# Kernel tuning notes

Hardware: AMD Instinct MI355X
Metric: run time of the kernel (lower is better)

## Reference

```python
import jax, jax.numpy as jnp
import numpy as np

S = 512      # seq_len -> S*S - S edges
V = 32000    # vocab_size
D = 128      # d_model
H = 4        # num_heads
L = 2        # num_layers
DN = 64      # d_node
DE = 64      # d_edge
DF = 4 * D   # ffn hidden
TEMP = 1.0   # temperature_init
E = S * S - S


def setup_inputs() -> dict:
    key = jax.random.key(0)
    ks = jax.random.split(key, 12)
    n = lambda k, shp: jax.random.normal(k, shp, dtype=jnp.float32) * 0.02
    return {
        "token_ids": jax.random.randint(ks[0], (S,), 0, V),
        "u": jax.random.uniform(ks[1], (E,), dtype=jnp.float32),
        "emb": n(ks[2], (V, D)),
        "Wqkv": n(ks[3], (L, D, 3 * D)), "bqkv": jnp.zeros((L, 3 * D)),
        "Wo": n(ks[4], (L, D, D)), "bo": jnp.zeros((L, D)),
        "ln1_g": jnp.ones((L, D)), "ln1_b": jnp.zeros((L, D)),
        "Wff1": n(ks[5], (L, D, DF)), "bff1": jnp.zeros((L, DF)),
        "Wff2": n(ks[6], (L, DF, D)), "bff2": jnp.zeros((L, D)),
        "ln2_g": jnp.ones((L, D)), "ln2_b": jnp.zeros((L, D)),
        "node_W": n(ks[7], (D, DN)), "node_b": jnp.zeros((DN,)),
        "sc_W1": n(ks[8], (2 * D + 1, D)), "sc_b1": jnp.zeros((D,)),
        "sc_W2": n(ks[9], (D, 1)), "sc_b2": jnp.zeros((1,)),
        "te_W": n(ks[10], (2 * D + 1, DE)), "te_b": jnp.zeros((DE,)),
    }


def _layernorm(x, g, b):
    m = jnp.mean(x, -1, keepdims=True)
    v = jnp.var(x, -1, keepdims=True)
    return (x - m) * jax.lax.rsqrt(v + 1e-5) * g + b


def _pos_encoding(s, d):
    pos = jnp.arange(s, dtype=jnp.float32)[:, None]
    div = jnp.exp(jnp.arange(0, d, 2, dtype=jnp.float32) * (-np.log(10000.0) / d))
    pe = jnp.zeros((s, d), dtype=jnp.float32)
    pe = pe.at[:, 0::2].set(jnp.sin(pos * div)).at[:, 1::2].set(jnp.cos(pos * div))
    return pe


_SRC_NP = np.repeat(np.arange(S), S)
_TGT_NP = np.tile(np.arange(S), S)
_KEEP = _SRC_NP != _TGT_NP
SRC = jnp.asarray(_SRC_NP[_KEEP])  # [E] static off-diagonal indices
TGT = jnp.asarray(_TGT_NP[_KEEP])


def _forward(token_ids, u, emb, Wqkv, bqkv, Wo, bo, ln1_g, ln1_b, Wff1, bff1,
             Wff2, bff2, ln2_g, ln2_b, node_W, node_b, sc_W1, sc_b1, sc_W2,
             sc_b2, te_W, te_b):
    # --- mini transformer backbone ---
    x = emb[token_ids] + _pos_encoding(S, D)  # [S, D]
    dh = D // H
    for l in range(L):
        qkv = x @ Wqkv[l] + bqkv[l]
        q, k, v = jnp.split(qkv, 3, axis=-1)
        q = q.reshape(S, H, dh); k = k.reshape(S, H, dh); v = v.reshape(S, H, dh)
        scores = jnp.einsum('qhd,khd->hqk', q, k) / np.sqrt(dh).astype(np.float32)
        attn = jax.nn.softmax(scores, axis=-1)
        o = jnp.einsum('hqk,khd->qhd', attn, v).reshape(S, D)
        x = _layernorm(x + o @ Wo[l] + bo[l], ln1_g[l], ln1_b[l])
        h = jax.nn.gelu(x @ Wff1[l] + bff1[l], approximate=False)
        x = _layernorm(x + h @ Wff2[l] + bff2[l], ln2_g[l], ln2_b[l])
    node_features = x @ node_W + node_b  # [S, DN]
    # --- all-pairs edge construction (off-diagonal) ---
    pos_diff = ((SRC - TGT).astype(jnp.float32) / S)[:, None]  # [E, 1]
    pair = jnp.concatenate([x[SRC], x[TGT], pos_diff], axis=-1)  # [E, 2D+1]
    # edge scorer MLP
    hs = jax.nn.gelu(pair @ sc_W1 + sc_b1, approximate=False)
    edge_logits = (hs @ sc_W2 + sc_b2)[:, 0]  # [E]
    # gumbel-sigmoid (soft, hard=False)
    uu = jnp.clip(u, 1e-8, 1.0 - 1e-8)
    gnoise = -jnp.log(-jnp.log(uu))
    edge_gates = jax.nn.sigmoid((edge_logits + gnoise) / TEMP)  # [E]
    # gated edge features
    edge_feats = (pair @ te_W + te_b) * edge_gates[:, None]  # [E, DE]
    return node_features, edge_feats, edge_gates


def reference(token_ids, u, emb, Wqkv, bqkv, Wo, bo, ln1_g, ln1_b, Wff1, bff1,
              Wff2, bff2, ln2_g, ln2_b, node_W, node_b, sc_W1, sc_b1, sc_W2,
              sc_b2, te_W, te_b):
    node_features, edge_feats, edge_gates = _forward(
        token_ids, u, emb, Wqkv, bqkv, Wo, bo, ln1_g, ln1_b, Wff1, bff1,
        Wff2, bff2, ln2_g, ln2_b, node_W, node_b, sc_W1, sc_b1, sc_W2,
        sc_b2, te_W, te_b)
    edge_index = jnp.stack([SRC, TGT])  # [2, E]
    return node_features, edge_feats, edge_index, edge_gates
```

## Files before the change

kernel.cpp:

```cpp
#include <hip/hip_runtime.h>
#include <math.h>

#define SS 512
#define DD 128
#define HH 4
#define DHH 32
#define DFF 512
#define E_EDGES 261632

__device__ __forceinline__ float gelu_f(float v) {
    return 0.5f * v * (1.0f + erff(v * 0.70710678118654752f));
}
__device__ __forceinline__ float fgelu(float x) {
    float x2 = x * x;
    float z = x * fmaf(-0.0713548164f, x2, -1.5957691216f);
    float e = __expf(z);
    return x * __builtin_amdgcn_rcpf(1.0f + e);
}

template<int DO_EMBED>
__global__ __launch_bounds__(384) void k_qkv(const float* __restrict__ xin,
                                             const int* __restrict__ tok,
                                             const float* __restrict__ emb,
                                             float* __restrict__ xout,
                                             const float* __restrict__ W,
                                             const float* __restrict__ b,
                                             float* __restrict__ qkv) {
    __shared__ float xs[DD];
    int row = blockIdx.x;
    int c = threadIdx.x;
    if (DO_EMBED) {
        if (c < 128) {
            float v = emb[(size_t)tok[row] * DD + c];
            int i2 = (c >> 1) << 1;
            float div = expf(-(float)i2 * (9.210340371976184f / 128.0f));
            float arg = (float)row * div;
            v += (c & 1) ? cosf(arg) : sinf(arg);
            xs[c] = v;
            xout[row * DD + c] = v;
        }
    } else {
        if (c < 128) xs[c] = xin[row * DD + c];
    }
    __syncthreads();
    float a = b[c];
    #pragma unroll 4
    for (int d = 0; d < DD; ++d) a = fmaf(xs[d], W[d * 384 + c], a);
    qkv[row * 384 + c] = a;
}

template<int DO_NODE>
__global__ __launch_bounds__(1024) void k_attn_tail(const float* __restrict__ qkv,
                                                    float* __restrict__ x,
                                                    const float* __restrict__ Wo,
                                                    const float* __restrict__ bo,
                                                    const float* __restrict__ g1,
                                                    const float* __restrict__ b1,
                                                    const float* __restrict__ W1,
                                                    const float* __restrict__ bf1,
                                                    const float* __restrict__ W2,
                                                    const float* __restrict__ bf2,
                                                    const float* __restrict__ g2,
                                                    const float* __restrict__ b2,
                                                    const float* __restrict__ nodeW,
                                                    const float* __restrict__ nodeb,
                                                    const float* __restrict__ scW1,
                                                    const float* __restrict__ scb1,
                                                    const float* __restrict__ teW,
                                                    const float* __restrict__ teb,
                                                    float* __restrict__ out_node,
                                                    float* __restrict__ As,
                                                    float* __restrict__ Atp,
                                                    float* __restrict__ Bs,
                                                    float* __restrict__ Btp) {
    int r0 = blockIdx.x * 2;
    int tid = threadIdx.x;
    int wave = tid >> 6, lane = tid & 63;
    __shared__ float sq[2][DD];
    __shared__ float ps[2][HH][SS];
    __shared__ float smax[2][HH][4], ssum[2][HH][4];
    __shared__ float opart[2][HH][4][DHH];
    __shared__ float os[2][DD];
    __shared__ float pred4[4][2][DD];
    __shared__ float x1[2][DD];
    __shared__ float hhl[2][DFF];
    __shared__ float xf[2][DD];
    __shared__ float red[2][2];
    if (tid < 256) sq[tid >> 7][tid & 127] = qkv[(r0 + (tid >> 7)) * 384 + (tid & 127)];
    __syncthreads();
    const float scale = 0.17677669529663687f;
    int h = wave & 3, kh = wave >> 2;
    int k0 = kh * 128 + lane, k1 = k0 + 64;
    float s00 = 0, s01 = 0, s10 = 0, s11 = 0;
    {
        const float4* kp0 = reinterpret_cast<const float4*>(&qkv[(size_t)k0 * 384 + 128 + h * DHH]);
        const float4* kp1 = reinterpret_cast<const float4*>(&qkv[(size_t)k1 * 384 + 128 + h * DHH]);
        #pragma unroll
        for (int i = 0; i < 8; ++i) {
            float4 a = kp0[i], bq = kp1[i];
            int d0 = h * DHH + i * 4;
            float q00 = sq[0][d0], q01 = sq[0][d0 + 1], q02 = sq[0][d0 + 2], q03 = sq[0][d0 + 3];
            float q10 = sq[1][d0], q11 = sq[1][d0 + 1], q12 = sq[1][d0 + 2], q13 = sq[1][d0 + 3];
            s00 += a.x * q00 + a.y * q01 + a.z * q02 + a.w * q03;
            s10 += a.x * q10 + a.y * q11 + a.z * q12 + a.w * q13;
            s01 += bq.x * q00 + bq.y * q01 + bq.z * q02 + bq.w * q03;
            s11 += bq.x * q10 + bq.y * q11 + bq.z * q12 + bq.w * q13;
        }
        s00 *= scale; s01 *= scale; s10 *= scale; s11 *= scale;
    }
    float m0 = fmaxf(s00, s01), m1 = fmaxf(s10, s11);
    for (int off = 32; off; off >>= 1) {
        m0 = fmaxf(m0, __shfl_xor(m0, off));
        m1 = fmaxf(m1, __shfl_xor(m1, off));
    }
    if (lane == 0) { smax[0][h][kh] = m0; smax[1][h][kh] = m1; }
    __syncthreads();
    float M0 = fmaxf(fmaxf(smax[0][h][0], smax[0][h][1]), fmaxf(smax[0][h][2], smax[0][h][3]));
    float M1 = fmaxf(fmaxf(smax[1][h][0], smax[1][h][1]), fmaxf(smax[1][h][2], smax[1][h][3]));
    float e00 = __expf(s00 - M0), e01 = __expf(s01 - M0);
    float e10 = __expf(s10 - M1), e11 = __expf(s11 - M1);
    float l0 = e00 + e01, l1 = e10 + e11;
    for (int off = 32; off; off >>= 1) {
        l0 += __shfl_xor(l0, off);
        l1 += __shfl_xor(l1, off);
    }
    if (lane == 0) { ssum[0][h][kh] = l0; ssum[1][h][kh] = l1; }
    __syncthreads();
    float inv0 = 1.0f / (ssum[0][h][0] + ssum[0][h][1] + ssum[0][h][2] + ssum[0][h][3]);
    float inv1 = 1.0f / (ssum[1][h][0] + ssum[1][h][1] + ssum[1][h][2] + ssum[1][h][3]);
    ps[0][h][k0] = e00 * inv0; ps[0][h][k1] = e01 * inv0;
    ps[1][h][k0] = e10 * inv1; ps[1][h][k1] = e11 * inv1;
    __syncthreads();
    {
        int hp = wave & 3, rp = (wave >> 2) & 1, khalf = wave >> 3;
        int d = lane & 31, sub = lane >> 5;
        int kbase = khalf * 256 + sub * 128;
        float acc = 0.f;
        #pragma unroll 4
        for (int i = 0; i < 128; ++i) {
            int ki = kbase + i;
            acc += ps[rp][hp][ki] * qkv[(size_t)ki * 384 + 256 + hp * DHH + d];
        }
        opart[rp][hp][khalf * 2 + sub][d] = acc;
    }
    __syncthreads();
    if (tid < 256) {
        int r = tid >> 7, cc = tid & 127;
        int h2 = cc >> 5, dd = cc & 31;
        os[r][cc] = opart[r][h2][0][dd] + opart[r][h2][1][dd] +
                    opart[r][h2][2][dd] + opart[r][h2][3][dd];
    }
    __syncthreads();
    int idx = tid & 255, kseg = tid >> 8;
    int rr = idx >> 7, cc2 = idx & 127;
    {
        float part = 0.f;
        #pragma unroll 8
        for (int q = 0; q < 32; ++q) {
            int dd = kseg * 32 + q;
            part = fmaf(os[rr][dd], Wo[dd * DD + cc2], part);
        }
        pred4[kseg][rr][cc2] = part;
    }
    __syncthreads();
    float val = pred4[0][rr][cc2] + pred4[1][rr][cc2] + pred4[2][rr][cc2] + pred4[3][rr][cc2]
              + x[(r0 + rr) * DD + cc2] + bo[cc2];
    int wig = (tid >> 6) & 1;
    float sum = val;
    for (int off = 32; off; off >>= 1) sum += __shfl_xor(sum, off);
    if (tid < 256 && (tid & 63) == 0) red[rr][wig] = sum;
    __syncthreads();
    float mean = (red[rr][0] + red[rr][1]) * (1.0f / 128.0f);
    float dv = val - mean;
    float sqv = dv * dv;
    for (int off = 32; off; off >>= 1) sqv += __shfl_xor(sqv, off);
    __syncthreads();
    if (tid < 256 && (tid & 63) == 0) red[rr][wig] = sqv;
    __syncthreads();
    float var = (red[rr][0] + red[rr][1]) * (1.0f / 128.0f);
    if (tid < 256) x1[rr][cc2] = dv * rsqrtf(var + 1e-5f) * g1[cc2] + b1[cc2];
    __syncthreads();
    {
        int rf = tid >> 9, cf = tid & 511;
        float s = bf1[cf];
        #pragma unroll 4
        for (int dd = 0; dd < DD; ++dd) s = fmaf(x1[rf][dd], W1[dd * DFF + cf], s);
        hhl[rf][cf] = gelu_f(s);
    }
    __syncthreads();
    {
        float p2 = 0.f;
        #pragma unroll 4
        for (int q = 0; q < 128; ++q) {
            int dd = kseg * 128 + q;
            p2 = fmaf(hhl[rr][dd], W2[dd * DD + cc2], p2);
        }
        pred4[kseg][rr][cc2] = p2;
    }
    __syncthreads();
    float val2 = pred4[0][rr][cc2] + pred4[1][rr][cc2] + pred4[2][rr][cc2] + pred4[3][rr][cc2]
               + x1[rr][cc2] + bf2[cc2];
    float sum2 = val2;
    for (int off = 32; off; off >>= 1) sum2 += __shfl_xor(sum2, off);
    if (tid < 256 && (tid & 63) == 0) red[rr][wig] = sum2;
    __syncthreads();
    float mean2 = (red[rr][0] + red[rr][1]) * (1.0f / 128.0f);
    float dv2 = val2 - mean2;
    float sq2 = dv2 * dv2;
    for (int off = 32; off; off >>= 1) sq2 += __shfl_xor(sq2, off);
    __syncthreads();
    if (tid < 256 && (tid & 63) == 0) red[rr][wig] = sq2;
    __syncthreads();
    float var2 = (red[rr][0] + red[rr][1]) * (1.0f / 128.0f);
    float outv = dv2 * rsqrtf(var2 + 1e-5f) * g2[cc2] + b2[cc2];
    if (!DO_NODE) {
        if (tid < 256) x[(r0 + rr) * DD + cc2] = outv;
        return;
    }
    if (tid < 256) xf[rr][cc2] = outv;
    __syncthreads();
    if (tid < 896) {
        int rl = (tid >= 448) ? 1 : 0;
        int cc = tid - rl * 448;
        int row = r0 + rl;
        const float* wp; int ldw; float bias = 0.f;
        if (cc < 64)       { wp = nodeW + cc;                     ldw = 64;  bias = nodeb[cc]; }
        else if (cc < 192) { wp = scW1 + (cc - 64);               ldw = 128; bias = scb1[cc - 64]; }
        else if (cc < 320) { wp = scW1 + 128 * 128 + (cc - 192);  ldw = 128; }
        else if (cc < 384) { wp = teW + (cc - 320);               ldw = 64;  bias = teb[cc - 320]; }
        else               { wp = teW + 128 * 64 + (cc - 384);    ldw = 64;  }
        float a = bias;
        #pragma unroll 4
        for (int dd = 0; dd < DD; ++dd) a = fmaf(xf[rl][dd], wp[dd * ldw], a);
        if (cc < 64)       out_node[row * 64 + cc] = a;
        else if (cc < 192) As[row * 128 + (cc - 64)] = a;
        else if (cc < 320) {
            int j0 = cc - 192;
            int hhi = j0 >> 6, rem = j0 & 63, jj = rem & 15, k = rem >> 4;
            Atp[row * 128 + jj * 8 + k * 2 + hhi] = a;
        }
        else if (cc < 384) Bs[row * 64 + (cc - 320)] = a;
        else {
            int jf = cc - 384, jj = jf & 15, k = jf >> 4;
            Btp[row * 64 + jj * 4 + k] = a;
        }
    }
}

__global__ __launch_bounds__(256) void k_edges(const float* __restrict__ As,
                                               const float* __restrict__ Atp,
                                               const float* __restrict__ Bs,
                                               const float* __restrict__ Btp,
                                               const float* __restrict__ scW1,
                                               const float* __restrict__ scW2,
                                               const float* __restrict__ scb2p,
                                               const float* __restrict__ teW,
                                               const float* __restrict__ u,
                                               float* __restrict__ out_feat,
                                               float* __restrict__ out_gate,
                                               float* __restrict__ out_ei) {
    int s = blockIdx.x;
    int seg = blockIdx.y;
    __shared__ float lAs[128], lap[128], lw2[128], lBs[64], lbp[64];
    int tid = threadIdx.x;
    if (tid < 128) {
        lAs[tid] = As[s * 128 + tid];
        lap[tid] = scW1[256 * 128 + tid];
        lw2[tid] = scW2[tid];
    } else if (tid < 192) {
        int j = tid - 128;
        lBs[j] = Bs[s * 64 + j];
        lbp[j] = teW[256 * 64 + j];
    }
    __syncthreads();
    int w = tid >> 6, lane = tid & 63;
    int g = lane >> 4, jj = lane & 15;
    float rAs[8], rap[8], rw2[8], rBs[4], rbp[4];
    #pragma unroll
    for (int k = 0; k < 4; ++k) {
        int j = jj + 16 * k;
        rAs[2 * k] = lAs[j]; rAs[2 * k + 1] = lAs[j + 64];
        rap[2 * k] = lap[j]; rap[2 * k + 1] = lap[j + 64];
        rw2[2 * k] = lw2[j]; rw2[2 * k + 1] = lw2[j + 64];
        rBs[k] = lBs[j]; rbp[k] = lbp[j];
    }
    float scb2 = scb2p[0];
    for (int iter = 0; iter < 16; ++iter) {
        int idx = seg * 256 + w * 64 + iter * 4 + g;
        if (idx >= 511) continue;
        int t = idx + (idx >= s);
        int e = s * 511 + idx;
        float pd = (float)(s - t) * (1.0f / 512.0f);
        const float4* ap = reinterpret_cast<const float4*>(&Atp[(size_t)t * 128 + jj * 8]);
        float4 at0 = ap[0];
        float4 at1 = ap[1];
        float part, a;
        a = fmaf(pd, rap[0], rAs[0] + at0.x); part  = fgelu(a) * rw2[0];
        a = fmaf(pd, rap[1], rAs[1] + at0.y); part += fgelu(a) * rw2[1];
        a = fmaf(pd, rap[2], rAs[2] + at0.z); part += fgelu(a) * rw2[2];
        a = fmaf(pd, rap[3], rAs[3] + at0.w); part += fgelu(a) * rw2[3];
        a = fmaf(pd, rap[4], rAs[4] + at1.x); part += fgelu(a) * rw2[4];
        a = fmaf(pd, rap[5], rAs[5] + at1.y); part += fgelu(a) * rw2[5];
        a = fmaf(pd, rap[6], rAs[6] + at1.z); part += fgelu(a) * rw2[6];
        a = fmaf(pd, rap[7], rAs[7] + at1.w); part += fgelu(a) * rw2[7];
        part += __shfl_xor(part, 1);
        part += __shfl_xor(part, 2);
        part += __shfl_xor(part, 4);
        part += __shfl_xor(part, 8);
        float logit = part + scb2;
        float uu = fminf(fmaxf(u[e], 1e-8f), 1.0f - 1e-8f);
        float nlv = -__logf(uu);
        float gate = __builtin_amdgcn_rcpf(1.0f + nlv * __expf(-logit));
        float4 bt = *reinterpret_cast<const float4*>(&Btp[(size_t)t * 64 + jj * 4]);
        float f0 = fmaf(pd, rbp[0], rBs[0] + bt.x) * gate;
        float f1 = fmaf(pd, rbp[1], rBs[1] + bt.y) * gate;
        float f2 = fmaf(pd, rbp[2], rBs[2] + bt.z) * gate;
        float f3 = fmaf(pd, rbp[3], rBs[3] + bt.w) * gate;
        size_t base = (size_t)e * 64 + jj;
        out_feat[base + 0]  = f0;
        out_feat[base + 16] = f1;
        out_feat[base + 32] = f2;
        out_feat[base + 48] = f3;
        if (jj == 0) { out_gate[e] = gate; out_ei[e] = (float)s; }
        else if (jj == 1) out_ei[E_EDGES + e] = (float)t;
    }
}

extern "C" void kernel_launch(void* const* d_in, const int* in_sizes, int n_in,
                              void* d_out, int out_size, void* d_ws, size_t ws_size,
                              hipStream_t stream) {
    const int*   tok   = (const int*)d_in[0];
    const float* u     = (const float*)d_in[1];
    const float* emb   = (const float*)d_in[2];
    const float* Wqkv  = (const float*)d_in[3];
    const float* bqkv  = (const float*)d_in[4];
    const float* Wo    = (const float*)d_in[5];
    const float* bo    = (const float*)d_in[6];
    const float* ln1g  = (const float*)d_in[7];
    const float* ln1b  = (const float*)d_in[8];
    const float* Wff1  = (const float*)d_in[9];
    const float* bff1  = (const float*)d_in[10];
    const float* Wff2  = (const float*)d_in[11];
    const float* bff2  = (const float*)d_in[12];
    const float* ln2g  = (const float*)d_in[13];
    const float* ln2b  = (const float*)d_in[14];
    const float* nodeW = (const float*)d_in[15];
    const float* nodeb = (const float*)d_in[16];
    const float* scW1  = (const float*)d_in[17];
    const float* scb1  = (const float*)d_in[18];
    const float* scW2  = (const float*)d_in[19];
    const float* scb2  = (const float*)d_in[20];
    const float* teW   = (const float*)d_in[21];
    const float* teb   = (const float*)d_in[22];

    float* out      = (float*)d_out;
    float* out_node = out;
    float* out_feat = out + 512 * 64;
    float* out_ei   = out_feat + (size_t)E_EDGES * 64;
    float* out_gate = out_ei + 2 * (size_t)E_EDGES;

    float* ws   = (float*)d_ws;
    float* x    = ws;
    float* qkv  = x + 512 * 128;
    float* As   = qkv + 512 * 384;
    float* Atp  = As + 512 * 128;
    float* Bs   = Atp + 512 * 128;
    float* Btp  = Bs + 512 * 64;

    k_qkv<1><<<dim3(512), dim3(384), 0, stream>>>(nullptr, tok, emb, x,
                                                  Wqkv, bqkv, qkv);
    k_attn_tail<0><<<dim3(256), dim3(1024), 0, stream>>>(qkv, x, Wo, bo,
                                                         ln1g, ln1b, Wff1, bff1, Wff2, bff2,
                                                         ln2g, ln2b,
                                                         nullptr, nullptr, nullptr, nullptr,
                                                         nullptr, nullptr,
                                                         nullptr, nullptr, nullptr, nullptr, nullptr);
    k_qkv<0><<<dim3(512), dim3(384), 0, stream>>>(x, nullptr, nullptr, nullptr,
                                                  Wqkv + 128 * 384, bqkv + 384, qkv);
    k_attn_tail<1><<<dim3(256), dim3(1024), 0, stream>>>(qkv, x, Wo + 128 * 128, bo + 128,
                                                         ln1g + 128, ln1b + 128,
                                                         Wff1 + 128 * 512, bff1 + 512,
                                                         Wff2 + 512 * 128, bff2 + 128,
                                                         ln2g + 128, ln2b + 128,
                                                         nodeW, nodeb, scW1, scb1, teW, teb,
                                                         out_node, As, Atp, Bs, Btp);
    k_edges<<<dim3(512, 2), dim3(256), 0, stream>>>(As, Atp, Bs, Btp, scW1, scW2, scb2, teW, u,
                                                    out_feat, out_gate, out_ei);
}
```

Before: 281.6 us.

## Process one row per attention-tail block and split edge kernel into more blocks

The attention/FFN tail kernel now handles one query row per 1024-thread block instead of two. The inner reductions (PV, Wo, FFN1, FFN2, node projections) are split across more K-segments with partial sums in shared memory, and the grid doubles to 512 blocks. The edge kernel grid is also doubled in its second dimension, with each block covering half as many target indices. The aim is more parallelism and shorter serial dot-product loops, at the cost of re-reading weights per row and more synchronisation per block.

```diff
diff --git a/kernel.cpp b/kernel.cpp
--- a/kernel.cpp
+++ b/kernel.cpp
@@ -50,199 +50,211 @@
 }
 
 template<int DO_NODE>
-__global__ __launch_bounds__(1024) void k_attn_tail(const float* __restrict__ qkv,
-                                                    float* __restrict__ x,
-                                                    const float* __restrict__ Wo,
-                                                    const float* __restrict__ bo,
-                                                    const float* __restrict__ g1,
-                                                    const float* __restrict__ b1,
-                                                    const float* __restrict__ W1,
-                                                    const float* __restrict__ bf1,
-                                                    const float* __restrict__ W2,
-                                                    const float* __restrict__ bf2,
-                                                    const float* __restrict__ g2,
-                                                    const float* __restrict__ b2,
-                                                    const float* __restrict__ nodeW,
-                                                    const float* __restrict__ nodeb,
-                                                    const float* __restrict__ scW1,
-                                                    const float* __restrict__ scb1,
-                                                    const float* __restrict__ teW,
-                                                    const float* __restrict__ teb,
-                                                    float* __restrict__ out_node,
-                                                    float* __restrict__ As,
-                                                    float* __restrict__ Atp,
-                                                    float* __restrict__ Bs,
-                                                    float* __restrict__ Btp) {
-    int r0 = blockIdx.x * 2;
+__global__ __launch_bounds__(1024, 8) void k_attn_tail(const float* __restrict__ qkv,
+                                                       float* __restrict__ x,
+                                                       const float* __restrict__ Wo,
+                                                       const float* __restrict__ bo,
+                                                       const float* __restrict__ g1,
+                                                       const float* __restrict__ b1,
+                                                       const float* __restrict__ W1,
+                                                       const float* __restrict__ bf1,
+                                                       const float* __restrict__ W2,
+                                                       const float* __restrict__ bf2,
+                                                       const float* __restrict__ g2,
+                                                       const float* __restrict__ b2,
+                                                       const float* __restrict__ nodeW,
+                                                       const float* __restrict__ nodeb,
+                                                       const float* __restrict__ scW1,
+                                                       const float* __restrict__ scb1,
+                                                       const float* __restrict__ teW,
+                                                       const float* __restrict__ teb,
+                                                       float* __restrict__ out_node,
+                                                       float* __restrict__ As,
+                                                       float* __restrict__ Atp,
+                                                       float* __restrict__ Bs,
+                                                       float* __restrict__ Btp) {
+    int r = blockIdx.x;
     int tid = threadIdx.x;
     int wave = tid >> 6, lane = tid & 63;
-    __shared__ float sq[2][DD];
-    __shared__ float ps[2][HH][SS];
-    __shared__ float smax[2][HH][4], ssum[2][HH][4];
-    __shared__ float opart[2][HH][4][DHH];
-    __shared__ float os[2][DD];
-    __shared__ float pred4[4][2][DD];
-    __shared__ float x1[2][DD];
-    __shared__ float hhl[2][DFF];
-    __shared__ float xf[2][DD];
-    __shared__ float red[2][2];
-    if (tid < 256) sq[tid >> 7][tid & 127] = qkv[(r0 + (tid >> 7)) * 384 + (tid & 127)];
+    __shared__ float sq[DD];
+    __shared__ float ps[HH][SS];
+    __shared__ float smax[HH][4], ssum[HH][4];
+    __shared__ float opart[HH][8][DHH];
+    __shared__ float os[DD];
+    __shared__ float pred8[8][DD];
+    __shared__ float x1s[DD];
+    __shared__ float f1p[2][DFF];
+    __shared__ float hhl[DFF];
+    __shared__ float xf[DD];
+    __shared__ float npart[2][448];
+    __shared__ float red[2], red2[2];
+    if (tid < DD) sq[tid] = qkv[r * 384 + tid];
     __syncthreads();
     const float scale = 0.17677669529663687f;
-    int h = wave & 3, kh = wave >> 2;
-    int k0 = kh * 128 + lane, k1 = k0 + 64;
-    float s00 = 0, s01 = 0, s10 = 0, s11 = 0;
+    int h = wave & 3, kq = wave >> 2;
+    int k0 = kq * 128 + lane, k1 = k0 + 64;
+    float s0 = 0.f, s1 = 0.f;
     {
         const float4* kp0 = reinterpret_cast<const float4*>(&qkv[(size_t)k0 * 384 + 128 + h * DHH]);
         const float4* kp1 = reinterpret_cast<const float4*>(&qkv[(size_t)k1 * 384 + 128 + h * DHH]);
         #pragma unroll
         for (int i = 0; i < 8; ++i) {
-            float4 a = kp0[i], bq = kp1[i];
+            float4 a = kp0[i], b4 = kp1[i];
             int d0 = h * DHH + i * 4;
-            float q00 = sq[0][d0], q01 = sq[0][d0 + 1], q02 = sq[0][d0 + 2], q03 = sq[0][d0 + 3];
-            float q10 = sq[1][d0], q11 = sq[1][d0 + 1], q12 = sq[1][d0 + 2], q13 = sq[1][d0 + 3];
-            s00 += a.x * q00 + a.y * q01 + a.z * q02 + a.w * q03;
-            s10 += a.x * q10 + a.y * q11 + a.z * q12 + a.w * q13;
-            s01 += bq.x * q00 + bq.y * q01 + bq.z * q02 + bq.w * q03;
-            s11 += bq.x * q10 + bq.y * q11 + bq.z * q12 + bq.w * q13;
-        }
-        s00 *= scale; s01 *= scale; s10 *= scale; s11 *= scale;
-    }
-    float m0 = fmaxf(s00, s01), m1 = fmaxf(s10, s11);
-    for (int off = 32; off; off >>= 1) {
-        m0 = fmaxf(m0, __shfl_xor(m0, off));
-        m1 = fmaxf(m1, __shfl_xor(m1, off));
-    }
-    if (lane == 0) { smax[0][h][kh] = m0; smax[1][h][kh] = m1; }
-    __syncthreads();
-    float M0 = fmaxf(fmaxf(smax[0][h][0], smax[0][h][1]), fmaxf(smax[0][h][2], smax[0][h][3]));
-    float M1 = fmaxf(fmaxf(smax[1][h][0], smax[1][h][1]), fmaxf(smax[1][h][2], smax[1][h][3]));
-    float e00 = __expf(s00 - M0), e01 = __expf(s01 - M0);
-    float e10 = __expf(s10 - M1), e11 = __expf(s11 - M1);
-    float l0 = e00 + e01, l1 = e10 + e11;
-    for (int off = 32; off; off >>= 1) {
-        l0 += __shfl_xor(l0, off);
-        l1 += __shfl_xor(l1, off);
-    }
-    if (lane == 0) { ssum[0][h][kh] = l0; ssum[1][h][kh] = l1; }
-    __syncthreads();
-    float inv0 = 1.0f / (ssum[0][h][0] + ssum[0][h][1] + ssum[0][h][2] + ssum[0][h][3]);
-    float inv1 = 1.0f / (ssum[1][h][0] + ssum[1][h][1] + ssum[1][h][2] + ssum[1][h][3]);
-    ps[0][h][k0] = e00 * inv0; ps[0][h][k1] = e01 * inv0;
-    ps[1][h][k0] = e10 * inv1; ps[1][h][k1] = e11 * inv1;
+            float q0 = sq[d0], q1 = sq[d0 + 1], q2 = sq[d0 + 2], q3 = sq[d0 + 3];
+            s0 += a.x * q0 + a.y * q1 + a.z * q2 + a.w * q3;
+            s1 += b4.x * q0 + b4.y * q1 + b4.z * q2 + b4.w * q3;
+        }
+        s0 *= scale; s1 *= scale;
+    }
+    float m = fmaxf(s0, s1);
+    for (int off = 32; off; off >>= 1) m = fmaxf(m, __shfl_xor(m, off));
+    if (lane == 0) smax[h][kq] = m;
+    __syncthreads();
+    float M = fmaxf(fmaxf(smax[h][0], smax[h][1]), fmaxf(smax[h][2], smax[h][3]));
+    float e0 = __expf(s0 - M), e1 = __expf(s1 - M);
+    float l = e0 + e1;
+    for (int off = 32; off; off >>= 1) l += __shfl_xor(l, off);
+    if (lane == 0) ssum[h][kq] = l;
+    __syncthreads();
+    float inv = 1.0f / (ssum[h][0] + ssum[h][1] + ssum[h][2] + ssum[h][3]);
+    ps[h][k0] = e0 * inv;
+    ps[h][k1] = e1 * inv;
     __syncthreads();
     {
-        int hp = wave & 3, rp = (wave >> 2) & 1, khalf = wave >> 3;
+        int hp = wave & 3, kq2 = wave >> 2;
         int d = lane & 31, sub = lane >> 5;
-        int kbase = khalf * 256 + sub * 128;
+        int kb = kq2 * 128 + sub * 64;
         float acc = 0.f;
-        #pragma unroll 4
-        for (int i = 0; i < 128; ++i) {
-            int ki = kbase + i;
-            acc += ps[rp][hp][ki] * qkv[(size_t)ki * 384 + 256 + hp * DHH + d];
-        }
-        opart[rp][hp][khalf * 2 + sub][d] = acc;
-    }
-    __syncthreads();
-    if (tid < 256) {
-        int r = tid >> 7, cc = tid & 127;
-        int h2 = cc >> 5, dd = cc & 31;
-        os[r][cc] = opart[r][h2][0][dd] + opart[r][h2][1][dd] +
-                    opart[r][h2][2][dd] + opart[r][h2][3][dd];
-    }
-    __syncthreads();
-    int idx = tid & 255, kseg = tid >> 8;
-    int rr = idx >> 7, cc2 = idx & 127;
+        #pragma unroll 8
+        for (int i = 0; i < 64; ++i) {
+            int ki = kb + i;
+            acc += ps[hp][ki] * qkv[(size_t)ki * 384 + 256 + hp * DHH + d];
+        }
+        opart[hp][kq2 * 2 + sub][d] = acc;
+    }
+    __syncthreads();
+    if (tid < DD) {
+        int h2 = tid >> 5, dd = tid & 31;
+        float o = 0.f;
+        #pragma unroll
+        for (int p = 0; p < 8; ++p) o += opart[h2][p][dd];
+        os[tid] = o;
+    }
+    __syncthreads();
+    int kseg = tid >> 7, cc = tid & 127;
     {
         float part = 0.f;
+        #pragma unroll
+        for (int q = 0; q < 16; ++q) {
+            int dd = kseg * 16 + q;
+            part = fmaf(os[dd], Wo[dd * DD + cc], part);
+        }
+        pred8[kseg][cc] = part;
+    }
+    __syncthreads();
+    float val = 0.f;
+    if (tid < DD) {
+        val = x[r * DD + tid] + bo[tid];
+        #pragma unroll
+        for (int p = 0; p < 8; ++p) val += pred8[p][tid];
+        float sum = val;
+        for (int off = 32; off; off >>= 1) sum += __shfl_xor(sum, off);
+        if (lane == 0) red[wave] = sum;
+    }
+    __syncthreads();
+    float mean = (red[0] + red[1]) * (1.0f / 128.0f);
+    float dv = val - mean;
+    if (tid < DD) {
+        float s2 = dv * dv;
+        for (int off = 32; off; off >>= 1) s2 += __shfl_xor(s2, off);
+        if (lane == 0) red2[wave] = s2;
+    }
+    __syncthreads();
+    float var = (red2[0] + red2[1]) * (1.0f / 128.0f);
+    if (tid < DD) x1s[tid] = dv * rsqrtf(var + 1e-5f) * g1[tid] + b1[tid];
+    __syncthreads();
+    {
+        int half = tid >> 9, cf = tid & 511;
+        float s = 0.f;
         #pragma unroll 8
-        for (int q = 0; q < 32; ++q) {
-            int dd = kseg * 32 + q;
-            part = fmaf(os[rr][dd], Wo[dd * DD + cc2], part);
-        }
-        pred4[kseg][rr][cc2] = part;
-    }
-    __syncthreads();
-    float val = pred4[0][rr][cc2] + pred4[1][rr][cc2] + pred4[2][rr][cc2] + pred4[3][rr][cc2]
-              + x[(r0 + rr) * DD + cc2] + bo[cc2];
-    int wig = (tid >> 6) & 1;
-    float sum = val;
-    for (int off = 32; off; off >>= 1) sum += __shfl_xor(sum, off);
-    if (tid < 256 && (tid & 63) == 0) red[rr][wig] = sum;
-    __syncthreads();
-    float mean = (red[rr][0] + red[rr][1]) * (1.0f / 128.0f);
-    float dv = val - mean;
-    float sqv = dv * dv;
-    for (int off = 32; off; off >>= 1) sqv += __shfl_xor(sqv, off);
-    __syncthreads();
-    if (tid < 256 && (tid & 63) == 0) red[rr][wig] = sqv;
-    __syncthreads();
-    float var = (red[rr][0] + red[rr][1]) * (1.0f / 128.0f);
-    if (tid < 256) x1[rr][cc2] = dv * rsqrtf(var + 1e-5f) * g1[cc2] + b1[cc2];
-    __syncthreads();
-    {
-        int rf = tid >> 9, cf = tid & 511;
-        float s = bf1[cf];
-        #pragma unroll 4
-        for (int dd = 0; dd < DD; ++dd) s = fmaf(x1[rf][dd], W1[dd * DFF + cf], s);
-        hhl[rf][cf] = gelu_f(s);
-    }
+        for (int q = 0; q < 64; ++q) {
+            int dd = half * 64 + q;
+            s = fmaf(x1s[dd], W1[dd * DFF + cf], s);
+        }
+        f1p[half][cf] = s;
+    }
+    __syncthreads();
+    if (tid < DFF) hhl[tid] = gelu_f(f1p[0][tid] + f1p[1][tid] + bf1[tid]);
     __syncthreads();
     {
         float p2 = 0.f;
-        #pragma unroll 4
-        for (int q = 0; q < 128; ++q) {
-            int dd = kseg * 128 + q;
-            p2 = fmaf(hhl[rr][dd], W2[dd * DD + cc2], p2);
-        }
-        pred4[kseg][rr][cc2] = p2;
-    }
-    __syncthreads();
-    float val2 = pred4[0][rr][cc2] + pred4[1][rr][cc2] + pred4[2][rr][cc2] + pred4[3][rr][cc2]
-               + x1[rr][cc2] + bf2[cc2];
-    float sum2 = val2;
-    for (int off = 32; off; off >>= 1) sum2 += __shfl_xor(sum2, off);
-    if (tid < 256 && (tid & 63) == 0) red[rr][wig] = sum2;
-    __syncthreads();
-    float mean2 = (red[rr][0] + red[rr][1]) * (1.0f / 128.0f);
+        #pragma unroll 8
+        for (int q = 0; q < 64; ++q) {
+            int dd = kseg * 64 + q;
+            p2 = fmaf(hhl[dd], W2[dd * DD + cc], p2);
+        }
+        pred8[kseg][cc] = p2;
+    }
+    __syncthreads();
+    float val2 = 0.f;
+    if (tid < DD) {
+        val2 = x1s[tid] + bf2[tid];
+        #pragma unroll
+        for (int p = 0; p < 8; ++p) val2 += pred8[p][tid];
+        float sum2 = val2;
+        for (int off = 32; off; off >>= 1) sum2 += __shfl_xor(sum2, off);
+        if (lane == 0) red[wave] = sum2;
+    }
+    __syncthreads();
+    float mean2 = (red[0] + red[1]) * (1.0f / 128.0f);
     float dv2 = val2 - mean2;
-    float sq2 = dv2 * dv2;
-    for (int off = 32; off; off >>= 1) sq2 += __shfl_xor(sq2, off);
-    __syncthreads();
-    if (tid < 256 && (tid & 63) == 0) red[rr][wig] = sq2;
-    __syncthreads();
-    float var2 = (red[rr][0] + red[rr][1]) * (1.0f / 128.0f);
-    float outv = dv2 * rsqrtf(var2 + 1e-5f) * g2[cc2] + b2[cc2];
+    if (tid < DD) {
+        float s2 = dv2 * dv2;
+        for (int off = 32; off; off >>= 1) s2 += __shfl_xor(s2, off);
+        if (lane == 0) red2[wave] = s2;
+    }
+    __syncthreads();
+    float var2 = (red2[0] + red2[1]) * (1.0f / 128.0f);
+    float outv = dv2 * rsqrtf(var2 + 1e-5f) * g2[tid & 127] + b2[tid & 127];
     if (!DO_NODE) {
-        if (tid < 256) x[(r0 + rr) * DD + cc2] = outv;
+        if (tid < DD) x[r * DD + tid] = outv;
         return;
     }
-    if (tid < 256) xf[rr][cc2] = outv;
+    if (tid < DD) xf[tid] = outv;
     __syncthreads();
     if (tid < 896) {
-        int rl = (tid >= 448) ? 1 : 0;
-        int cc = tid - rl * 448;
-        int row = r0 + rl;
-        const float* wp; int ldw; float bias = 0.f;
-        if (cc < 64)       { wp = nodeW + cc;                     ldw = 64;  bias = nodeb[cc]; }
-        else if (cc < 192) { wp = scW1 + (cc - 64);               ldw = 128; bias = scb1[cc - 64]; }
-        else if (cc < 320) { wp = scW1 + 128 * 128 + (cc - 192);  ldw = 128; }
-        else if (cc < 384) { wp = teW + (cc - 320);               ldw = 64;  bias = teb[cc - 320]; }
-        else               { wp = teW + 128 * 64 + (cc - 384);    ldw = 64;  }
-        float a = bias;
-        #pragma unroll 4
-        for (int dd = 0; dd < DD; ++dd) a = fmaf(xf[rl][dd], wp[dd * ldw], a);
-        if (cc < 64)       out_node[row * 64 + cc] = a;
-        else if (cc < 192) As[row * 128 + (cc - 64)] = a;
-        else if (cc < 320) {
-            int j0 = cc - 192;
+        int half = (tid >= 448) ? 1 : 0;
+        int cc2 = tid - half * 448;
+        const float* wp; int ldw;
+        if (cc2 < 64)       { wp = nodeW + cc2;                     ldw = 64;  }
+        else if (cc2 < 192) { wp = scW1 + (cc2 - 64);               ldw = 128; }
+        else if (cc2 < 320) { wp = scW1 + 128 * 128 + (cc2 - 192);  ldw = 128; }
+        else if (cc2 < 384) { wp = teW + (cc2 - 320);               ldw = 64;  }
+        else                { wp = teW + 128 * 64 + (cc2 - 384);    ldw = 64;  }
+        float a = 0.f;
+        #pragma unroll 8
+        for (int q = 0; q < 64; ++q) {
+            int dd = half * 64 + q;
+            a = fmaf(xf[dd], wp[dd * ldw], a);
+        }
+        npart[half][cc2] = a;
+    }
+    __syncthreads();
+    if (tid < 448) {
+        int cc2 = tid;
+        float a = npart[0][cc2] + npart[1][cc2];
+        if (cc2 < 64)       out_node[r * 64 + cc2] = a + nodeb[cc2];
+        else if (cc2 < 192) As[r * 128 + (cc2 - 64)] = a + scb1[cc2 - 64];
+        else if (cc2 < 320) {
+            int j0 = cc2 - 192;
             int hhi = j0 >> 6, rem = j0 & 63, jj = rem & 15, k = rem >> 4;
-            Atp[row * 128 + jj * 8 + k * 2 + hhi] = a;
-        }
-        else if (cc < 384) Bs[row * 64 + (cc - 320)] = a;
+            Atp[r * 128 + jj * 8 + k * 2 + hhi] = a;
+        }
+        else if (cc2 < 384) Bs[r * 64 + (cc2 - 320)] = a + teb[cc2 - 320];
         else {
-            int jf = cc - 384, jj = jf & 15, k = jf >> 4;
-            Btp[row * 64 + jj * 4 + k] = a;
+            int jf = cc2 - 384, jj = jf & 15, k = jf >> 4;
+            Btp[r * 64 + jj * 4 + k] = a;
         }
     }
 }
@@ -285,8 +297,8 @@
         rBs[k] = lBs[j]; rbp[k] = lbp[j];
     }
     float scb2 = scb2p[0];
-    for (int iter = 0; iter < 16; ++iter) {
-        int idx = seg * 256 + w * 64 + iter * 4 + g;
+    for (int iter = 0; iter < 8; ++iter) {
+        int idx = seg * 128 + iter * 16 + w * 4 + g;
         if (idx >= 511) continue;
         int t = idx + (idx >= s);
         int e = s * 511 + idx;
@@ -369,7 +381,7 @@
 
     k_qkv<1><<<dim3(512), dim3(384), 0, stream>>>(nullptr, tok, emb, x,
                                                   Wqkv, bqkv, qkv);
-    k_attn_tail<0><<<dim3(256), dim3(1024), 0, stream>>>(qkv, x, Wo, bo,
+    k_attn_tail<0><<<dim3(512), dim3(1024), 0, stream>>>(qkv, x, Wo, bo,
                                                          ln1g, ln1b, Wff1, bff1, Wff2, bff2,
                                                          ln2g, ln2b,
                                                          nullptr, nullptr, nullptr, nullptr,
@@ -377,13 +389,13 @@
                                                          nullptr, nullptr, nullptr, nullptr, nullptr);
     k_qkv<0><<<dim3(512), dim3(384), 0, stream>>>(x, nullptr, nullptr, nullptr,
                                                   Wqkv + 128 * 384, bqkv + 384, qkv);
-    k_attn_tail<1><<<dim3(256), dim3(1024), 0, stream>>>(qkv, x, Wo + 128 * 128, bo + 128,
+    k_attn_tail<1><<<dim3(512), dim3(1024), 0, stream>>>(qkv, x, Wo + 128 * 128, bo + 128,
                                                          ln1g + 128, ln1b + 128,
                                                          Wff1 + 128 * 512, bff1 + 512,
                                                          Wff2 + 512 * 128, bff2 + 128,
                                                          ln2g + 128, ln2b + 128,
                                                          nodeW, nodeb, scW1, scb1, teW, teb,
                                                          out_node, As, Atp, Bs, Btp);
-    k_edges<<<dim3(512, 2), dim3(256), 0, stream>>>(As, Atp, Bs, Btp, scW1, scW2, scb2, teW, u,
+    k_edges<<<dim3(512, 4), dim3(256), 0, stream>>>(As, Atp, Bs, Btp, scW1, scW2, scb2, teW, u,
                                                     out_feat, out_gate, out_ei);
 }
```

Result: faster. 258.7 us (-8.1%).
